# Optimization experiments

Hardware: AMD Instinct MI355X
Metric: run time of the kernel (lower is better)

Reference implementation:

```python
import jax, jax.numpy as jnp
import numpy as np

N_HEADS = 16
LN_EPS = 1e-5


def setup_inputs() -> dict:
    key = jax.random.key(0)
    k_z, k_qkv, k_proj = jax.random.split(key, 3)
    b, n, dm = 4, 2048, 1024
    z = jax.random.normal(k_z, (b, n, dm), dtype=jnp.float32)
    gamma = jnp.ones((dm,), dtype=jnp.float32)
    beta = jnp.zeros((dm,), dtype=jnp.float32)
    # parameterize Linear weights as (in, out) so y = x @ w (same math as torch x @ W.T)
    w_qkv = jax.random.normal(k_qkv, (dm, 3 * dm), dtype=jnp.float32) * (1.0 / np.sqrt(dm))
    w_proj = jax.random.normal(k_proj, (dm, dm), dtype=jnp.float32) * (1.0 / np.sqrt(dm))
    b_proj = jnp.zeros((dm,), dtype=jnp.float32)
    return {"z": z, "gamma": gamma, "beta": beta, "w_qkv": w_qkv,
            "w_proj": w_proj, "b_proj": b_proj}


def reference(z, gamma, beta, w_qkv, w_proj, b_proj):
    b, n, dm = z.shape
    h = N_HEADS
    d = dm // h
    scaling = jnp.asarray(np.sqrt(dm / h), dtype=z.dtype)

    # LayerNorm over last dim
    mu = jnp.mean(z, axis=-1, keepdims=True)
    var = jnp.mean(jnp.square(z - mu), axis=-1, keepdims=True)
    zn = (z - mu) * jax.lax.rsqrt(var + LN_EPS) * gamma + beta

    qkv = zn @ w_qkv  # [b, n, 3*dm]
    # einops 'b n (h d qkv_n) -> qkv_n b h n d': qkv index is INNERMOST of packed dim
    qkv = qkv.reshape(b, n, h, d, 3)
    q = qkv[..., 0]  # [b, n, h, d]
    k = qkv[..., 1]
    v = qkv[..., 2]

    scores = jnp.einsum('bqhd,bkhd->bhqk', q, k) / scaling  # [b, h, n, n]
    att = jax.nn.softmax(scores, axis=-1)
    out = jnp.einsum('bhqk,bkhd->bqhd', att, v).reshape(b, n, dm)
    out = out @ w_proj + b_proj  # projection (drop_hidden=False); dropout is identity in eval
    return z + out
```

## Files before the change

### kernel.cpp

```cpp
#include <hip/hip_runtime.h>

typedef unsigned short ushort;
typedef unsigned int uint;

typedef __bf16 bf16x8 __attribute__((ext_vector_type(8)));
typedef float floatx4 __attribute__((ext_vector_type(4)));

constexpr int BATCH = 4;
constexpr int SEQ = 2048;
constexpr int DM = 1024;
constexpr int NH = 16;
constexpr int HD = 64;
constexpr int M = BATCH * SEQ;
constexpr int NQKV = 3 * DM;
constexpr float QSCALE = 0.18033688011112042f;

__device__ __forceinline__ ushort f2b(float f) {
    uint x; __builtin_memcpy(&x, &f, 4);
    x += 0x7fffu + ((x >> 16) & 1u);
    return (ushort)(x >> 16);
}

__device__ __forceinline__ void gload16(const ushort* g, ushort* l) {
    __builtin_amdgcn_global_load_lds(
        (const __attribute__((address_space(1))) void*)g,
        (__attribute__((address_space(3))) void*)l, 16, 0, 0);
}

__global__ __launch_bounds__(256) void transpose_cast(
    const float* __restrict__ in, ushort* __restrict__ out, int R, int C) {
    __shared__ ushort tile[64][65];
    int c0 = blockIdx.x * 64, r0 = blockIdx.y * 64;
    int tx = threadIdx.x & 63, ty = threadIdx.x >> 6;
#pragma unroll
    for (int i = 0; i < 64; i += 4)
        tile[i + ty][tx] = f2b(in[(size_t)(r0 + i + ty) * C + c0 + tx]);
    __syncthreads();
#pragma unroll
    for (int i = 0; i < 64; i += 4)
        out[(size_t)(c0 + i + ty) * R + r0 + tx] = tile[tx][i + ty];
}

__global__ __launch_bounds__(256) void transpose_cast_qkv(
    const float* __restrict__ in, ushort* __restrict__ out) {
    __shared__ ushort tile[64][65];
    int c0 = blockIdx.x * 64, r0 = blockIdx.y * 64;
    int tx = threadIdx.x & 63, ty = threadIdx.x >> 6;
#pragma unroll
    for (int i = 0; i < 64; i += 4)
        tile[i + ty][tx] = f2b(in[(size_t)(r0 + i + ty) * NQKV + c0 + tx]);
    __syncthreads();
#pragma unroll
    for (int i = 0; i < 64; i += 4) {
        int c = c0 + i + ty;
        int cp = (c % 3) * DM + c / 3;
        out[(size_t)cp * DM + r0 + tx] = tile[tx][i + ty];
    }
}

__global__ __launch_bounds__(256) void ln_kernel(
    const float* __restrict__ z, const float* __restrict__ gamma,
    const float* __restrict__ beta, ushort* __restrict__ zn) {
    int row = blockIdx.x;
    int t = threadIdx.x;
    float4 v = reinterpret_cast<const float4*>(z + (size_t)row * DM)[t];
    float s = v.x + v.y + v.z + v.w;
    float sq = v.x * v.x + v.y * v.y + v.z * v.z + v.w * v.w;
#pragma unroll
    for (int off = 32; off >= 1; off >>= 1) {
        s  += __shfl_xor(s, off);
        sq += __shfl_xor(sq, off);
    }
    __shared__ float red[8];
    int wave = t >> 6;
    if ((t & 63) == 0) { red[wave] = s; red[wave + 4] = sq; }
    __syncthreads();
    s  = red[0] + red[1] + red[2] + red[3];
    sq = red[4] + red[5] + red[6] + red[7];
    float mean = s * (1.f / DM);
    float var  = sq * (1.f / DM) - mean * mean;
    float rstd = rsqrtf(var + 1e-5f);
    float4 g = reinterpret_cast<const float4*>(gamma)[t];
    float4 bt = reinterpret_cast<const float4*>(beta)[t];
    ushort4 o;
    o.x = f2b((v.x - mean) * rstd * g.x + bt.x);
    o.y = f2b((v.y - mean) * rstd * g.y + bt.y);
    o.z = f2b((v.z - mean) * rstd * g.z + bt.z);
    o.w = f2b((v.w - mean) * rstd * g.w + bt.w);
    reinterpret_cast<ushort4*>(zn + (size_t)row * DM)[t] = o;
}

__device__ __forceinline__ void gemm128_core(
    const ushort* __restrict__ A, const ushort* __restrict__ BT,
    int m0, int n0, int t, floatx4 (&acc)[4][4],
    ushort (*As)[64], ushort (*Bs)[64]) {
    int lane = t & 63, w = t >> 6;
    int l16 = lane & 15, quad = lane >> 4;
    int wm = (w >> 1) * 64, wn = (w & 1) * 64;
#pragma unroll
    for (int i = 0; i < 4; i++)
#pragma unroll
        for (int j = 0; j < 4; j++) acc[i][j] = (floatx4){0.f, 0.f, 0.f, 0.f};

    int srow8 = lane >> 3;
    int lseg = (lane & 7) ^ srow8;
    const ushort* gA[4]; const ushort* gB[4];
    ushort* lA[4]; ushort* lB[4];
#pragma unroll
    for (int c = 0; c < 4; c++) {
        int r = 32 * c + 8 * w + srow8;
        gA[c] = &A [(size_t)(m0 + r) * DM + lseg * 8];
        gB[c] = &BT[(size_t)(n0 + r) * DM + lseg * 8];
        lA[c] = &As[32 * c + 8 * w][0];
        lB[c] = &Bs[32 * c + 8 * w][0];
    }
    int sw = l16 & 7;

    for (int k0 = 0; k0 < DM; k0 += 64) {
#pragma unroll
        for (int c = 0; c < 4; c++) {
            gload16(gA[c] + k0, lA[c]);
            gload16(gB[c] + k0, lB[c]);
        }
        __syncthreads();
#pragma unroll
        for (int kk = 0; kk < 2; kk++) {
            bf16x8 af[4], bf[4];
#pragma unroll
            for (int i = 0; i < 4; i++)
                af[i] = *reinterpret_cast<const bf16x8*>(
                    &As[wm + i * 16 + l16][((kk * 4 + quad) ^ sw) << 3]);
#pragma unroll
            for (int j = 0; j < 4; j++)
                bf[j] = *reinterpret_cast<const bf16x8*>(
                    &Bs[wn + j * 16 + l16][((kk * 4 + quad) ^ sw) << 3]);
#pragma unroll
            for (int i = 0; i < 4; i++)
#pragma unroll
                for (int j = 0; j < 4; j++)
                    acc[i][j] = __builtin_amdgcn_mfma_f32_16x16x32_bf16(
                        af[i], bf[j], acc[i][j], 0, 0, 0);
        }
        __syncthreads();
    }
}

__global__ __launch_bounds__(256) void gemm_qkv(
    const ushort* __restrict__ A,
    const ushort* __restrict__ BT,
    ushort* __restrict__ Q, ushort* __restrict__ K, ushort* __restrict__ V) {
    __shared__ ushort smem[16384];
    ushort (*As)[64] = (ushort(*)[64])smem;
    ushort (*Bs)[64] = (ushort(*)[64])(smem + 8192);
    ushort* Cs = smem;
    int t = threadIdx.x;
    int m0 = blockIdx.y * 128, n0 = blockIdx.x * 128;
    floatx4 acc[4][4];
    gemm128_core(A, BT, m0, n0, t, acc, As, Bs);
    int lane = t & 63, w = t >> 6;
    int l16 = lane & 15, quad = lane >> 4;
    int wn = (w & 1) * 64;
    int which = n0 >> 10;
    int hd0 = n0 & 1023;
    float scale = (which == 0) ? QSCALE : 1.0f;
    int bb = m0 >> 11;
    int nb = m0 & 2047;
    ushort* dstQK = (which == 0) ? Q : K;

#pragma unroll
    for (int p = 0; p < 2; p++) {
        __syncthreads();
        if ((w >> 1) == p) {
            if (which < 2) {
#pragma unroll
                for (int i = 0; i < 4; i++)
#pragma unroll
                    for (int j = 0; j < 4; j++)
#pragma unroll
                        for (int r = 0; r < 4; r++)
                            Cs[(i * 16 + quad * 4 + r) * 136 + wn + j * 16 + l16] =
                                f2b(acc[i][j][r] * scale);
            } else {
#pragma unroll
                for (int i = 0; i < 4; i++)
#pragma unroll
                    for (int j = 0; j < 4; j++)
#pragma unroll
                        for (int r = 0; r < 4; r++)
                            Cs[(wn + j * 16 + l16) * 72 + i * 16 + quad * 4 + r] =
                                f2b(acc[i][j][r]);
            }
        }
        __syncthreads();
        if (which < 2) {
            int ch = (t & 15) * 8;
#pragma unroll
            for (int u = 0; u < 4; u++) {
                int lr = (t >> 4) + u * 16;
                int n = nb + p * 64 + lr;
                int hh = (hd0 + ch) >> 6, dd = ch & 63;
                *reinterpret_cast<uint4*>(
                    &dstQK[((size_t)((bb * NH + hh) * SEQ) + n) * HD + dd]) =
                    *reinterpret_cast<const uint4*>(&Cs[lr * 136 + ch]);
            }
        } else {
            int nch = (t & 7) * 8;
#pragma unroll
            for (int u = 0; u < 4; u++) {
                int dc = (t >> 3) + u * 32;
                int hh = (hd0 >> 6) + (dc >> 6), dd = dc & 63;
                int n = nb + p * 64 + nch;
                *reinterpret_cast<uint4*>(
                    &V[((size_t)((bb * NH + hh) * HD) + dd) * SEQ + n]) =
                    *reinterpret_cast<const uint4*>(&Cs[dc * 72 + nch]);
            }
        }
    }
}

__global__ __launch_bounds__(256) void gemm_proj(
    const ushort* __restrict__ A,
    const ushort* __restrict__ BT,
    const float* __restrict__ bias, const float* __restrict__ z,
    float* __restrict__ out) {
    __shared__ ushort As[128][64];
    __shared__ ushort Bs[128][64];
    int t = threadIdx.x;
    int m0 = blockIdx.y * 128, n0 = blockIdx.x * 128;
    floatx4 acc[4][4];
    gemm128_core(A, BT, m0, n0, t, acc, As, Bs);
    int lane = t & 63, w = t >> 6;
    int l16 = lane & 15, quad = lane >> 4;
    int wm = (w >> 1) * 64, wn = (w & 1) * 64;
#pragma unroll
    for (int j = 0; j < 4; j++) {
        int col = n0 + wn + j * 16 + l16;
        float bz = bias[col];
#pragma unroll
        for (int i = 0; i < 4; i++) {
#pragma unroll
            for (int r = 0; r < 4; r++) {
                int row = m0 + wm + i * 16 + quad * 4 + r;
                out[(size_t)row * DM + col] =
                    acc[i][j][r] + bz + z[(size_t)row * DM + col];
            }
        }
    }
}

__global__ __launch_bounds__(256) void attn_kernel(
    const ushort* __restrict__ Q, const ushort* __restrict__ K,
    const ushort* __restrict__ Vt, ushort* __restrict__ O) {
    __shared__ ushort QsPs[128 * 64];
    __shared__ ushort Ks[64 * 64];
    __shared__ ushort Vs[64 * 64];
    int t = threadIdx.x;
    int lane = t & 63, w = t >> 6;
    int l16 = lane & 15, quad = lane >> 4;
    int id = blockIdx.x;
    int qt = id >> 6, bh = id & 63;
    int bb = bh >> 4, h = bh & 15;
    int q0 = qt * 128;
    const ushort* Qg = Q  + (size_t)((bb * NH + h) * SEQ + q0) * HD;
    const ushort* Kg = K  + (size_t)((bb * NH + h) * SEQ) * HD;
    const ushort* Vg = Vt + (size_t)((bb * NH + h) * HD) * SEQ;

    int srow = lane >> 3;
    int lseg = (lane & 7) ^ srow;
    int r0 = 8 * w + srow;

    gload16(Qg + (size_t)r0 * HD + lseg * 8,         &QsPs[w * 512]);
    gload16(Qg + (size_t)(32 + r0) * HD + lseg * 8,  &QsPs[2048 + w * 512]);
    gload16(Qg + (size_t)(64 + r0) * HD + lseg * 8,  &QsPs[4096 + w * 512]);
    gload16(Qg + (size_t)(96 + r0) * HD + lseg * 8,  &QsPs[6144 + w * 512]);
    gload16(Kg + (size_t)r0 * HD + lseg * 8,         &Ks[w * 512]);
    gload16(Kg + (size_t)(32 + r0) * HD + lseg * 8,  &Ks[2048 + w * 512]);
    gload16(Vg + (size_t)r0 * SEQ + lseg * 8,        &Vs[w * 512]);
    gload16(Vg + (size_t)(32 + r0) * SEQ + lseg * 8, &Vs[2048 + w * 512]);
    __syncthreads();

    int swl = l16 & 7;
    bf16x8 aq[2][2];
    ushort* PsRow[2];
#pragma unroll
    for (int g = 0; g < 2; g++) {
        int row = 32 * w + 16 * g + l16;
        aq[g][0] = *reinterpret_cast<const bf16x8*>(&QsPs[row * 64 + ((quad ^ swl) << 3)]);
        aq[g][1] = *reinterpret_cast<const bf16x8*>(&QsPs[row * 64 + (((quad + 4) ^ swl) << 3)]);
        PsRow[g] = &QsPs[row * 64];
    }

    size_t koff1 = (size_t)r0 * HD + lseg * 8;
    size_t koff2 = (size_t)(32 + r0) * HD + lseg * 8;
    size_t voff1 = (size_t)r0 * SEQ + lseg * 8;
    size_t voff2 = (size_t)(32 + r0) * SEQ + lseg * 8;
    ushort* kw1 = &Ks[w * 512 + (lane & 63) * 8];
    ushort* kw2 = &Ks[2048 + w * 512 + (lane & 63) * 8];
    ushort* vw1 = &Vs[w * 512 + (lane & 63) * 8];
    ushort* vw2 = &Vs[2048 + w * 512 + (lane & 63) * 8];
    const ushort* Kp = Kg + (size_t)64 * HD;
    const ushort* Vp = Vg + 64;

    bf16x8 bones;
    {
        union { ushort u[8]; bf16x8 v; } cvt;
        ushort one = (l16 == 0) ? (ushort)0x3F80 : (ushort)0;
#pragma unroll
        for (int i = 0; i < 8; i++) cvt.u[i] = one;
        bones = cvt.v;
    }

    floatx4 Oacc[2][4], lacc[2];
#pragma unroll
    for (int g = 0; g < 2; g++) {
        lacc[g] = (floatx4){0.f, 0.f, 0.f, 0.f};
#pragma unroll
        for (int tt = 0; tt < 4; tt++) Oacc[g][tt] = (floatx4){0.f, 0.f, 0.f, 0.f};
    }

    constexpr int NT = SEQ / 64;
    for (int kt = 0; kt < NT; kt++) {
        uint4 kr1 = *reinterpret_cast<const uint4*>(Kp + koff1);
        uint4 kr2 = *reinterpret_cast<const uint4*>(Kp + koff2);
        uint4 vr1 = *reinterpret_cast<const uint4*>(Vp + voff1);
        uint4 vr2 = *reinterpret_cast<const uint4*>(Vp + voff2);
        Kp += (size_t)64 * HD;
        Vp += 64;

        floatx4 sacc[2][4];
#pragma unroll
        for (int nt = 0; nt < 4; nt++) {
            bf16x8 ak0 = *reinterpret_cast<const bf16x8*>(&Ks[(nt * 16 + l16) * 64 + ((quad ^ swl) << 3)]);
            bf16x8 ak1 = *reinterpret_cast<const bf16x8*>(&Ks[(nt * 16 + l16) * 64 + (((quad + 4) ^ swl) << 3)]);
#pragma unroll
            for (int g = 0; g < 2; g++) {
                floatx4 sv = (floatx4){0.f, 0.f, 0.f, 0.f};
                sv = __builtin_amdgcn_mfma_f32_16x16x32_bf16(ak0, aq[g][0], sv, 0, 0, 0);
                sv = __builtin_amdgcn_mfma_f32_16x16x32_bf16(ak1, aq[g][1], sv, 0, 0, 0);
                sacc[g][nt] = sv;
            }
        }
#pragma unroll
        for (int g = 0; g < 2; g++) {
#pragma unroll
            for (int nt = 0; nt < 4; nt++) {
                float p0 = __builtin_amdgcn_exp2f(sacc[g][nt][0]);
                float p1 = __builtin_amdgcn_exp2f(sacc[g][nt][1]);
                float p2 = __builtin_amdgcn_exp2f(sacc[g][nt][2]);
                float p3 = __builtin_amdgcn_exp2f(sacc[g][nt][3]);
                uint b0, b1, b2, b3;
                __builtin_memcpy(&b0, &p0, 4); __builtin_memcpy(&b1, &p1, 4);
                __builtin_memcpy(&b2, &p2, 4); __builtin_memcpy(&b3, &p3, 4);
                uint2 pk;
                pk.x = __builtin_amdgcn_perm(b1, b0, 0x07060302u);
                pk.y = __builtin_amdgcn_perm(b3, b2, 0x07060302u);
                int lseg2 = 2 * nt + (quad >> 1);
                *reinterpret_cast<uint2*>(&PsRow[g][((lseg2 ^ swl) << 3) + (quad & 1) * 4]) = pk;
            }
        }
#pragma unroll
        for (int ks = 0; ks < 2; ks++) {
            bf16x8 ap[2];
#pragma unroll
            for (int g = 0; g < 2; g++) {
                ap[g] = *reinterpret_cast<const bf16x8*>(
                    &PsRow[g][(((4 * ks + quad) ^ swl) << 3)]);
                lacc[g] = __builtin_amdgcn_mfma_f32_16x16x32_bf16(ap[g], bones, lacc[g], 0, 0, 0);
            }
#pragma unroll
            for (int tt = 0; tt < 4; tt++) {
                bf16x8 bv = *reinterpret_cast<const bf16x8*>(
                    &Vs[(tt * 16 + l16) * 64 + ((((ks * 4 + quad)) ^ swl) << 3)]);
#pragma unroll
                for (int g = 0; g < 2; g++)
                    Oacc[g][tt] = __builtin_amdgcn_mfma_f32_16x16x32_bf16(ap[g], bv, Oacc[g][tt], 0, 0, 0);
            }
        }
        __syncthreads();
        *reinterpret_cast<uint4*>(kw1) = kr1;
        *reinterpret_cast<uint4*>(kw2) = kr2;
        *reinterpret_cast<uint4*>(vw1) = vr1;
        *reinterpret_cast<uint4*>(vw2) = vr2;
        __syncthreads();
    }
    float lq[2][4];
#pragma unroll
    for (int g = 0; g < 2; g++)
#pragma unroll
        for (int j = 0; j < 4; j++) lq[g][j] = __shfl(lacc[g][j], quad << 4);

#pragma unroll
    for (int g = 0; g < 2; g++) {
#pragma unroll
        for (int tt = 0; tt < 4; tt++) {
#pragma unroll
            for (int j = 0; j < 4; j++) {
                int n = q0 + 32 * w + 16 * g + quad * 4 + j;
                int dcol = tt * 16 + l16;
                float val = Oacc[g][tt][j] / lq[g][j];
                O[(size_t)(bb * SEQ + n) * DM + h * HD + dcol] = f2b(val);
            }
        }
    }
}

extern "C" void kernel_launch(void* const* d_in, const int* in_sizes, int n_in,
                              void* d_out, int out_size, void* d_ws, size_t ws_size,
                              hipStream_t stream) {
    const float* z      = (const float*)d_in[0];
    const float* gamma  = (const float*)d_in[1];
    const float* beta   = (const float*)d_in[2];
    const float* w_qkv  = (const float*)d_in[3];
    const float* w_proj = (const float*)d_in[4];
    const float* b_proj = (const float*)d_in[5];
    float* out = (float*)d_out;

    char* ws = (char*)d_ws;
    const size_t SZ = (size_t)M * DM * sizeof(ushort);
    ushort* zn   = (ushort*)(ws);
    ushort* Qb   = (ushort*)(ws + SZ);
    ushort* Kb   = (ushort*)(ws + 2 * SZ);
    ushort* Vb   = (ushort*)(ws + 3 * SZ);
    ushort* wqT  = (ushort*)(ws + 4 * SZ);
    ushort* wpT  = (ushort*)(ws + 4 * SZ + (size_t)DM * NQKV * sizeof(ushort));
    ushort* Ob = zn;

    dim3 tq(NQKV / 64, DM / 64);
    transpose_cast_qkv<<<tq, 256, 0, stream>>>(w_qkv, wqT);
    dim3 tp(DM / 64, DM / 64);
    transpose_cast<<<tp, 256, 0, stream>>>(w_proj, wpT, DM, DM);
    ln_kernel<<<M, 256, 0, stream>>>(z, gamma, beta, zn);
    dim3 g1(NQKV / 128, M / 128);
    gemm_qkv<<<g1, 256, 0, stream>>>(zn, wqT, Qb, Kb, Vb);
    attn_kernel<<<(SEQ / 128) * BATCH * NH, 256, 0, stream>>>(Qb, Kb, Vb, Ob);
    dim3 g3(DM / 128, M / 128);
    gemm_proj<<<g3, 256, 0, stream>>>(Ob, wpT, b_proj, z, out);
}
```

Baseline: 277.9 us.

## Merge weight transposes and layernorm into one prep launch; remap GEMM block order

Combines the two weight transpose-cast kernels and the layernorm kernel into a single launch that dispatches on block index, removing two kernel launches and their serialization gaps. GEMM grids become 1D with the M tile index in the fastest-varying bits, so consecutive blocks share the same weight column tile and reuse it in cache. The merged kernel allocates the transpose shared tile for layernorm blocks too, which may slightly reduce occupancy there.

Result: faster. 268.8 us (-3.3%).

```diff
diff --git a/kernel.cpp b/kernel.cpp
--- a/kernel.cpp
+++ b/kernel.cpp
@@ -27,42 +27,43 @@
         (__attribute__((address_space(3))) void*)l, 16, 0, 0);
 }
 
-__global__ __launch_bounds__(256) void transpose_cast(
-    const float* __restrict__ in, ushort* __restrict__ out, int R, int C) {
-    __shared__ ushort tile[64][65];
-    int c0 = blockIdx.x * 64, r0 = blockIdx.y * 64;
-    int tx = threadIdx.x & 63, ty = threadIdx.x >> 6;
-#pragma unroll
-    for (int i = 0; i < 64; i += 4)
-        tile[i + ty][tx] = f2b(in[(size_t)(r0 + i + ty) * C + c0 + tx]);
-    __syncthreads();
-#pragma unroll
-    for (int i = 0; i < 64; i += 4)
-        out[(size_t)(c0 + i + ty) * R + r0 + tx] = tile[tx][i + ty];
-}
-
-__global__ __launch_bounds__(256) void transpose_cast_qkv(
-    const float* __restrict__ in, ushort* __restrict__ out) {
-    __shared__ ushort tile[64][65];
-    int c0 = blockIdx.x * 64, r0 = blockIdx.y * 64;
-    int tx = threadIdx.x & 63, ty = threadIdx.x >> 6;
-#pragma unroll
-    for (int i = 0; i < 64; i += 4)
-        tile[i + ty][tx] = f2b(in[(size_t)(r0 + i + ty) * NQKV + c0 + tx]);
-    __syncthreads();
-#pragma unroll
-    for (int i = 0; i < 64; i += 4) {
-        int c = c0 + i + ty;
-        int cp = (c % 3) * DM + c / 3;
-        out[(size_t)cp * DM + r0 + tx] = tile[tx][i + ty];
-    }
-}
-
-__global__ __launch_bounds__(256) void ln_kernel(
+__global__ __launch_bounds__(256) void prep_kernel(
+    const float* __restrict__ w_qkv, ushort* __restrict__ wqT,
+    const float* __restrict__ w_proj, ushort* __restrict__ wpT,
     const float* __restrict__ z, const float* __restrict__ gamma,
     const float* __restrict__ beta, ushort* __restrict__ zn) {
-    int row = blockIdx.x;
+    __shared__ ushort tile[64][65];
+    int id = blockIdx.x;
     int t = threadIdx.x;
+    if (id < 1024) {
+        int tx = t & 63, ty = t >> 6;
+        if (id < 768) {
+            int bx = id % 48, by = id / 48;
+            int c0 = bx * 64, r0 = by * 64;
+#pragma unroll
+            for (int i = 0; i < 64; i += 4)
+                tile[i + ty][tx] = f2b(w_qkv[(size_t)(r0 + i + ty) * NQKV + c0 + tx]);
+            __syncthreads();
+#pragma unroll
+            for (int i = 0; i < 64; i += 4) {
+                int c = c0 + i + ty;
+                int cp = (c % 3) * DM + c / 3;
+                wqT[(size_t)cp * DM + r0 + tx] = tile[tx][i + ty];
+            }
+        } else {
+            int q = id - 768;
+            int c0 = (q % 16) * 64, r0 = (q / 16) * 64;
+#pragma unroll
+            for (int i = 0; i < 64; i += 4)
+                tile[i + ty][tx] = f2b(w_proj[(size_t)(r0 + i + ty) * DM + c0 + tx]);
+            __syncthreads();
+#pragma unroll
+            for (int i = 0; i < 64; i += 4)
+                wpT[(size_t)(c0 + i + ty) * DM + r0 + tx] = tile[tx][i + ty];
+        }
+        return;
+    }
+    int row = id - 1024;
     float4 v = reinterpret_cast<const float4*>(z + (size_t)row * DM)[t];
     float s = v.x + v.y + v.z + v.w;
     float sq = v.x * v.x + v.y * v.y + v.z * v.z + v.w * v.w;
@@ -154,7 +155,8 @@
     ushort (*Bs)[64] = (ushort(*)[64])(smem + 8192);
     ushort* Cs = smem;
     int t = threadIdx.x;
-    int m0 = blockIdx.y * 128, n0 = blockIdx.x * 128;
+    int id = blockIdx.x;
+    int m0 = (id & 63) * 128, n0 = (id >> 6) * 128;
     floatx4 acc[4][4];
     gemm128_core(A, BT, m0, n0, t, acc, As, Bs);
     int lane = t & 63, w = t >> 6;
@@ -226,7 +228,8 @@
     __shared__ ushort As[128][64];
     __shared__ ushort Bs[128][64];
     int t = threadIdx.x;
-    int m0 = blockIdx.y * 128, n0 = blockIdx.x * 128;
+    int id = blockIdx.x;
+    int m0 = (id & 63) * 128, n0 = (id >> 6) * 128;
     floatx4 acc[4][4];
     gemm128_core(A, BT, m0, n0, t, acc, As, Bs);
     int lane = t & 63, w = t >> 6;
@@ -425,14 +428,9 @@
     ushort* wpT  = (ushort*)(ws + 4 * SZ + (size_t)DM * NQKV * sizeof(ushort));
     ushort* Ob = zn;
 
-    dim3 tq(NQKV / 64, DM / 64);
-    transpose_cast_qkv<<<tq, 256, 0, stream>>>(w_qkv, wqT);
-    dim3 tp(DM / 64, DM / 64);
-    transpose_cast<<<tp, 256, 0, stream>>>(w_proj, wpT, DM, DM);
-    ln_kernel<<<M, 256, 0, stream>>>(z, gamma, beta, zn);
-    dim3 g1(NQKV / 128, M / 128);
-    gemm_qkv<<<g1, 256, 0, stream>>>(zn, wqT, Qb, Kb, Vb);
+    prep_kernel<<<1024 + M, 256, 0, stream>>>(w_qkv, wqT, w_proj, wpT,
+                                              z, gamma, beta, zn);
+    gemm_qkv<<<(NQKV / 128) * 64, 256, 0, stream>>>(zn, wqT, Qb, Kb, Vb);
     attn_kernel<<<(SEQ / 128) * BATCH * NH, 256, 0, stream>>>(Qb, Kb, Vb, Ob);
-    dim3 g3(DM / 128, M / 128);
-    gemm_proj<<<g3, 256, 0, stream>>>(Ob, wpT, b_proj, z, out);
-}
+    gemm_proj<<<(DM / 128) * 64, 256, 0, stream>>>(Ob, wpT, b_proj, z, out);
+}
```
